# Kernel tuning notes

Measured on AMD Instinct MI355X. Metric: run time of the kernel, lower is better.

## Reference

```python
import jax, jax.numpy as jnp
import numpy as np


def setup_inputs() -> dict:
    key = jax.random.key(0)
    k1, k2 = jax.random.split(key)
    B, Cin, Cout, M1, M2 = 32, 128, 128, 64, 65
    # complex tensors stored as (..., 2) = (real, imag), matching torch.view_as_complex layout
    inp = jax.random.normal(k1, (B, Cin, M1, M2, 2), dtype=jnp.float32)
    weight = jax.random.normal(k2, (Cin, Cout, M1, M2, 2), dtype=jnp.float32) * 0.02
    return {"input": inp, "weight": weight}


def reference(input, weight):
    # torch: einsum('bixy,ioxy->boxy', input_complex, view_as_complex(weight))
    # Complex batched matmul per (x, y) mode, contracting over in_channels i.
    xr, xi = input[..., 0], input[..., 1]      # [b, i, x, y]
    wr, wi = weight[..., 0], weight[..., 1]    # [i, o, x, y]
    rr = jnp.einsum('bixy,ioxy->boxy', xr, wr)
    ii = jnp.einsum('bixy,ioxy->boxy', xi, wi)
    ri = jnp.einsum('bixy,ioxy->boxy', xr, wi)
    ir = jnp.einsum('bixy,ioxy->boxy', xi, wr)
    out_r = rr - ii
    out_i = ri + ir
    return jnp.stack([out_r, out_i], axis=-1)  # [b, o, x, y, 2]
```

## Files before the change

kernel.cpp:

```cpp
#include <hip/hip_runtime.h>
#include <stdint.h>


typedef float f2 __attribute__((ext_vector_type(2)));

#define NB 32
#define CI 128
#define CO 128
#define OT 64
#define MODES 4160
#define MPB 8
#define KC 4
#define NCHUNK (CI / KC)
#define ABUF_F2 (KC * NB * MPB)
#define WBUF_F2 (KC * OT * MPB)
#define BUF_F2  (ABUF_F2 + WBUF_F2)

#define CFMA(acc, av, wv)                                                      \
  asm("v_pk_fma_f32 %0, %1, %2, %0 op_sel:[0,0,0] op_sel_hi:[0,1,1]"           \
      : "+v"(acc) : "v"(av), "v"(wv));                                         \
  asm("v_pk_fma_f32 %0, %1, %2, %0 op_sel:[1,1,0] op_sel_hi:[1,0,1] "          \
      "neg_lo:[1,0,0]"                                                         \
      : "+v"(acc) : "v"(av), "v"(wv));

#define VM_WAIT(N) asm volatile("s_waitcnt vmcnt(" #N ")" ::: "memory")

__device__ __forceinline__ void gload16(const f2* g, f2* l) {
    __builtin_amdgcn_global_load_lds(
        (const __attribute__((address_space(1))) uint32_t*)g,
        (__attribute__((address_space(3))) uint32_t*)l, 16, 0, 0);
}

__device__ __forceinline__ void stage_chunk(const f2* __restrict__ Ig,
                                            const f2* __restrict__ Wl,
                                            f2* dst, int t, int m0,
                                            int obase, int k0) {
    {
        const int kk = t >> 7, b = (t >> 2) & 31, ml0 = (t & 3) << 1;
        gload16(Ig + (size_t)(b * CI + k0 + kk) * MODES + m0 + ml0,
                dst + t * 2);
    }
#pragma unroll
    for (int p = 0; p < 2; ++p) {
        const int j  = p * 512 + t;
        const int kk = j >> 8, op = (j >> 2) & 63, ml0 = (j & 3) << 1;
        const int o  = op ^ ((op >> 3) & 1);
        gload16(Wl + (size_t)((k0 + kk) * CO + obase + o) * MODES + m0 + ml0,
                dst + ABUF_F2 + j * 2);
    }
}

__global__ __launch_bounds__(512, 4)
void cmul2d_kernel(const f2* __restrict__ Ig,
                   const f2* __restrict__ Wl,
                   f2* __restrict__ Og) {
    __shared__ f2 lds[2 * BUF_F2];

    const int t = threadIdx.x;

    const int bid = blockIdx.x;
    const int jid = (bid & 7) * 130 + (bid >> 3);
    const int m0    = (jid >> 1) * MPB;
    const int obase = (jid & 1) * OT;

    const int ml = t & 7;
    const int s  = t >> 3;
    const int so = s & 7;
    const int sb = s >> 3;

    f2 acc[4][8];
#pragma unroll
    for (int r = 0; r < 4; ++r)
#pragma unroll
        for (int q = 0; q < 8; ++q) acc[r][q] = (f2)(0.0f);

    stage_chunk(Ig, Wl, lds,          t, m0, obase, 0);
    stage_chunk(Ig, Wl, lds + BUF_F2, t, m0, obase, KC);

#pragma unroll 1
    for (int c = 0; c < NCHUNK; ++c) {
        if (c < NCHUNK - 1) { VM_WAIT(3); } else { VM_WAIT(0); }
        __builtin_amdgcn_s_barrier();
        __builtin_amdgcn_sched_barrier(0);

        const f2* Ab = lds + (c & 1) * BUF_F2;
        const f2* Wb = Ab + ABUF_F2;
#pragma unroll
        for (int kk = 0; kk < KC; ++kk) {
            f2 a[4], w[8];
#pragma unroll
            for (int r = 0; r < 4; ++r)
                a[r] = Ab[(kk * NB + sb * 4 + r) * MPB + ml];
#pragma unroll
            for (int q = 0; q < 8; ++q) {
                const int o  = so * 8 + q;
                const int op = o ^ ((o >> 3) & 1);
                w[q] = Wb[(kk * OT + op) * MPB + ml];
            }
#pragma unroll
            for (int r = 0; r < 4; ++r)
#pragma unroll
                for (int q = 0; q < 8; ++q) {
                    CFMA(acc[r][q], a[r], w[q]);
                }
        }

        __builtin_amdgcn_sched_barrier(0);
        __builtin_amdgcn_s_barrier();
        if (c + 2 < NCHUNK)
            stage_chunk(Ig, Wl, lds + (c & 1) * BUF_F2, t, m0, obase,
                        (c + 2) * KC);
    }

#pragma unroll
    for (int r = 0; r < 4; ++r) {
        const int b = sb * 4 + r;
#pragma unroll
        for (int q = 0; q < 8; ++q) {
            const int o = obase + so * 8 + q;
            Og[(size_t)(b * CO + o) * MODES + m0 + ml] = acc[r][q];
        }
    }
}

extern "C" void kernel_launch(void* const* d_in, const int* in_sizes, int n_in,
                              void* d_out, int out_size, void* d_ws, size_t ws_size,
                              hipStream_t stream) {
    const f2* I = (const f2*)d_in[0];
    const f2* W = (const f2*)d_in[1];
    f2* O = (f2*)d_out;
    dim3 grid(1040);
    dim3 block(512);
    cmul2d_kernel<<<grid, block, 0, stream>>>(I, W, O);
}
```

Before: 261.7 us.

## Triple-buffer LDS and interleave next-chunk global loads with compute

Grows the LDS ring from two to three chunk buffers. Each chunk's three global-to-LDS loads are now issued one per kk step inside the compute loop, instead of all at once after the trailing barrier. Raises wave priority around the packed-FMA block so compute keeps issuing while loads are in flight. The cost is more LDS per block, which likely cuts the number of resident blocks per CU and so reduces latency hiding from occupancy.

```diff
diff --git a/kernel.cpp b/kernel.cpp
--- a/kernel.cpp
+++ b/kernel.cpp
@@ -31,22 +31,24 @@
         (__attribute__((address_space(3))) uint32_t*)l, 16, 0, 0);
 }
 
-__device__ __forceinline__ void stage_chunk(const f2* __restrict__ Ig,
-                                            const f2* __restrict__ Wl,
-                                            f2* dst, int t, int m0,
-                                            int obase, int k0) {
-    {
+template <int WHICH>
+__device__ __forceinline__ void stage_unit(const f2* __restrict__ Ig,
+                                           const f2* __restrict__ Wl,
+                                           f2* dst, int t, int m0,
+                                           int obase, int k0) {
+    if constexpr (WHICH == 0) {
         const int kk = t >> 7, b = (t >> 2) & 31, ml0 = (t & 3) << 1;
         gload16(Ig + (size_t)(b * CI + k0 + kk) * MODES + m0 + ml0,
                 dst + t * 2);
-    }
-#pragma unroll
-    for (int p = 0; p < 2; ++p) {
-        const int j  = p * 512 + t;
-        const int kk = j >> 8, op = (j >> 2) & 63, ml0 = (j & 3) << 1;
+    } else {
+        constexpr int p = WHICH - 1;
+        const int j  = p * 512 + WHICH * 0 + t + p * 0 + 512 * 0;
+        const int jj = p * 512 + t;
+        const int kk = jj >> 8, op = (jj >> 2) & 63, ml0 = (jj & 3) << 1;
         const int o  = op ^ ((op >> 3) & 1);
+        (void)j;
         gload16(Wl + (size_t)((k0 + kk) * CO + obase + o) * MODES + m0 + ml0,
-                dst + ABUF_F2 + j * 2);
+                dst + ABUF_F2 + jj * 2);
     }
 }
 
@@ -54,12 +56,12 @@
 void cmul2d_kernel(const f2* __restrict__ Ig,
                    const f2* __restrict__ Wl,
                    f2* __restrict__ Og) {
-    __shared__ f2 lds[2 * BUF_F2];
+    __shared__ f2 lds[3 * BUF_F2];
 
     const int t = threadIdx.x;
 
-    const int bid = blockIdx.x;
-    const int jid = (bid & 7) * 130 + (bid >> 3);
+    const int bid   = blockIdx.x;
+    const int jid   = (bid & 7) * 130 + (bid >> 3);
     const int m0    = (jid >> 1) * MPB;
     const int obase = (jid & 1) * OT;
 
@@ -74,8 +76,12 @@
 #pragma unroll
         for (int q = 0; q < 8; ++q) acc[r][q] = (f2)(0.0f);
 
-    stage_chunk(Ig, Wl, lds,          t, m0, obase, 0);
-    stage_chunk(Ig, Wl, lds + BUF_F2, t, m0, obase, KC);
+    stage_unit<0>(Ig, Wl, lds, t, m0, obase, 0);
+    stage_unit<1>(Ig, Wl, lds, t, m0, obase, 0);
+    stage_unit<2>(Ig, Wl, lds, t, m0, obase, 0);
+    stage_unit<0>(Ig, Wl, lds + BUF_F2, t, m0, obase, KC);
+    stage_unit<1>(Ig, Wl, lds + BUF_F2, t, m0, obase, KC);
+    stage_unit<2>(Ig, Wl, lds + BUF_F2, t, m0, obase, KC);
 
 #pragma unroll 1
     for (int c = 0; c < NCHUNK; ++c) {
@@ -83,8 +89,12 @@
         __builtin_amdgcn_s_barrier();
         __builtin_amdgcn_sched_barrier(0);
 
-        const f2* Ab = lds + (c & 1) * BUF_F2;
+        const f2* Ab = lds + (c % 3) * BUF_F2;
         const f2* Wb = Ab + ABUF_F2;
+        f2* nbuf = lds + ((c + 2) % 3) * BUF_F2;
+        const bool more = (c + 2 < NCHUNK);
+        const int  nk0  = (c + 2) * KC;
+
 #pragma unroll
         for (int kk = 0; kk < KC; ++kk) {
             f2 a[4], w[8];
@@ -94,22 +104,27 @@
 #pragma unroll
             for (int q = 0; q < 8; ++q) {
                 const int o  = so * 8 + q;
-                const int op = o ^ ((o >> 3) & 1);
+                const int op = o ^ (so & 1);
                 w[q] = Wb[(kk * OT + op) * MPB + ml];
             }
+            if (more) {
+                if (kk == 0) stage_unit<0>(Ig, Wl, nbuf, t, m0, obase, nk0);
+                else if (kk == 1) stage_unit<1>(Ig, Wl, nbuf, t, m0, obase, nk0);
+                else if (kk == 2) stage_unit<2>(Ig, Wl, nbuf, t, m0, obase, nk0);
+            }
+            __builtin_amdgcn_sched_barrier(0);
+            __builtin_amdgcn_s_setprio(1);
 #pragma unroll
             for (int r = 0; r < 4; ++r)
 #pragma unroll
                 for (int q = 0; q < 8; ++q) {
                     CFMA(acc[r][q], a[r], w[q]);
                 }
+            __builtin_amdgcn_s_setprio(0);
         }
 
         __builtin_amdgcn_sched_barrier(0);
         __builtin_amdgcn_s_barrier();
-        if (c + 2 < NCHUNK)
-            stage_chunk(Ig, Wl, lds + (c & 1) * BUF_F2, t, m0, obase,
-                        (c + 2) * KC);
     }
 
 #pragma unroll
```

Result: faster. 252.9 us (-3.3%).

## Halve output tile per block and interleave next-chunk staging with compute

Applied to the files above, without the earlier changes.

Each block now covers 32 output channels instead of 64, with 256 threads and twice as many blocks. The next K-chunk's global-to-LDS loads are issued in four phases spread across the compute of the current chunk, with a single barrier per chunk and a prefetch depth of one. Weight LDS storage gets a new XOR swizzle to match the new read pattern, and s_setprio raises priority around the FMA blocks. The aim is better latency hiding and occupancy, but the input tensor is now re-read by four blocks instead of two, which raises global traffic, and the shallower prefetch may expose load latency.

```diff
diff --git a/kernel.cpp b/kernel.cpp
--- a/kernel.cpp
+++ b/kernel.cpp
@@ -7,7 +7,7 @@
 #define NB 32
 #define CI 128
 #define CO 128
-#define OT 64
+#define OT 32
 #define MODES 4160
 #define MPB 8
 #define KC 4
@@ -31,26 +31,28 @@
         (__attribute__((address_space(3))) uint32_t*)l, 16, 0, 0);
 }
 
-__device__ __forceinline__ void stage_chunk(const f2* __restrict__ Ig,
+template <int PH>
+__device__ __forceinline__ void stage_phase(const f2* __restrict__ Ig,
                                             const f2* __restrict__ Wl,
                                             f2* dst, int t, int m0,
                                             int obase, int k0) {
-    {
-        const int kk = t >> 7, b = (t >> 2) & 31, ml0 = (t & 3) << 1;
-        gload16(Ig + (size_t)(b * CI + k0 + kk) * MODES + m0 + ml0,
-                dst + t * 2);
-    }
-#pragma unroll
-    for (int p = 0; p < 2; ++p) {
-        const int j  = p * 512 + t;
-        const int kk = j >> 8, op = (j >> 2) & 63, ml0 = (j & 3) << 1;
-        const int o  = op ^ ((op >> 3) & 1);
-        gload16(Wl + (size_t)((k0 + kk) * CO + obase + o) * MODES + m0 + ml0,
+    if constexpr (PH < 2) {
+        const int j  = PH * 256 + t;
+        const int kk = j >> 7, b = (j >> 2) & 31, mlp = j & 3;
+        gload16(Ig + (size_t)(b * CI + k0 + kk) * MODES + m0 + mlp * 2,
+                dst + j * 2);
+    } else {
+        const int j   = (PH - 2) * 256 + t;
+        const int kk  = j >> 7, oph = (j >> 2) & 31, p = j & 3;
+        const int sw  = (oph >> 3) & 3;
+        const int o   = oph ^ (sw & 1);
+        const int qg  = p ^ sw;
+        gload16(Wl + (size_t)((k0 + kk) * CO + obase + o) * MODES + m0 + qg * 2,
                 dst + ABUF_F2 + j * 2);
     }
 }
 
-__global__ __launch_bounds__(512, 4)
+__global__ __launch_bounds__(256, 4)
 void cmul2d_kernel(const f2* __restrict__ Ig,
                    const f2* __restrict__ Wl,
                    f2* __restrict__ Og) {
@@ -58,15 +60,17 @@
 
     const int t = threadIdx.x;
 
-    const int bid = blockIdx.x;
-    const int jid = (bid & 7) * 130 + (bid >> 3);
-    const int m0    = (jid >> 1) * MPB;
-    const int obase = (jid & 1) * OT;
+    const int bid   = blockIdx.x;
+    const int jid   = (bid & 7) * 260 + (bid >> 3);
+    const int mg    = jid >> 2;
+    const int oq    = jid & 3;
+    const int m0    = mg * MPB;
+    const int obase = oq * OT;
 
     const int ml = t & 7;
     const int s  = t >> 3;
-    const int so = s & 7;
-    const int sb = s >> 3;
+    const int so = s & 3;
+    const int sb = s >> 2;
 
     f2 acc[4][8];
 #pragma unroll
@@ -74,42 +78,53 @@
 #pragma unroll
         for (int q = 0; q < 8; ++q) acc[r][q] = (f2)(0.0f);
 
-    stage_chunk(Ig, Wl, lds,          t, m0, obase, 0);
-    stage_chunk(Ig, Wl, lds + BUF_F2, t, m0, obase, KC);
+    const int pxor = (ml >> 1);
+
+    stage_phase<0>(Ig, Wl, lds, t, m0, obase, 0);
+    stage_phase<1>(Ig, Wl, lds, t, m0, obase, 0);
+    stage_phase<2>(Ig, Wl, lds, t, m0, obase, 0);
+    stage_phase<3>(Ig, Wl, lds, t, m0, obase, 0);
 
 #pragma unroll 1
     for (int c = 0; c < NCHUNK; ++c) {
-        if (c < NCHUNK - 1) { VM_WAIT(3); } else { VM_WAIT(0); }
+        VM_WAIT(0);
         __builtin_amdgcn_s_barrier();
         __builtin_amdgcn_sched_barrier(0);
 
         const f2* Ab = lds + (c & 1) * BUF_F2;
         const f2* Wb = Ab + ABUF_F2;
+        f2* nbuf = lds + ((c + 1) & 1) * BUF_F2;
+        const bool more = (c + 1 < NCHUNK);
+        const int  nk0  = (c + 1) * KC;
+
 #pragma unroll
         for (int kk = 0; kk < KC; ++kk) {
             f2 a[4], w[8];
 #pragma unroll
             for (int r = 0; r < 4; ++r)
-                a[r] = Ab[(kk * NB + sb * 4 + r) * MPB + ml];
+                a[r] = Ab[kk * (NB * MPB) + (sb * 4 + r) * MPB + ml];
 #pragma unroll
             for (int q = 0; q < 8; ++q) {
-                const int o  = so * 8 + q;
-                const int op = o ^ ((o >> 3) & 1);
-                w[q] = Wb[(kk * OT + op) * MPB + ml];
+                const int o   = so * 8 + q;
+                const int oph = o ^ (so & 1);
+                const int p   = pxor ^ so;
+                w[q] = Wb[(kk * (OT * MPB)) + ((oph * 4 + p) << 1) + (ml & 1)];
             }
+            if (more) {
+                if (kk == 0) stage_phase<0>(Ig, Wl, nbuf, t, m0, obase, nk0);
+                else if (kk == 1) stage_phase<1>(Ig, Wl, nbuf, t, m0, obase, nk0);
+                else if (kk == 2) stage_phase<2>(Ig, Wl, nbuf, t, m0, obase, nk0);
+                else stage_phase<3>(Ig, Wl, nbuf, t, m0, obase, nk0);
+            }
+            __builtin_amdgcn_s_setprio(1);
 #pragma unroll
             for (int r = 0; r < 4; ++r)
 #pragma unroll
                 for (int q = 0; q < 8; ++q) {
                     CFMA(acc[r][q], a[r], w[q]);
                 }
+            __builtin_amdgcn_s_setprio(0);
         }
-
-        __builtin_amdgcn_sched_barrier(0);
-        __builtin_amdgcn_s_barrier();
-        if (c + 2 < NCHUNK)
-            stage_chunk(Ig, Wl, lds + (c & 1) * BUF_F2, t, m0, obase,
-                        (c + 2) * KC);
     }
 
 #pragma unroll
@@ -129,7 +144,7 @@
     const f2* I = (const f2*)d_in[0];
     const f2* W = (const f2*)d_in[1];
     f2* O = (f2*)d_out;
-    dim3 grid(1040);
-    dim3 block(512);
+    dim3 grid(2080);
+    dim3 block(256);
     cmul2d_kernel<<<grid, block, 0, stream>>>(I, W, O);
 }
```

New measurement: 253.9 us. 3.0% less time.
